# Kernel tuning notes

Hardware: AMD Instinct MI355X
Metric: run time of the kernel (lower is better)

## Reference

```python
import jax, jax.numpy as jnp
import numpy as np

N = 50000
E = 800000
NODE_DIM = 15
HID = 64
HEADS = 4
NEG_SLOPE = 0.2


def _add_self_loops(edge_index, n):
    loops = jnp.arange(n, dtype=edge_index.dtype)
    src = jnp.concatenate([edge_index[0], loops])
    dst = jnp.concatenate([edge_index[1], loops])
    return src, dst


def gat_conv(x, edge_index, W, att_src, att_dst, bias, concat):
    # x: [N, F_in]; W: [F_in, heads*out]; att_*: [heads, out]; bias: [heads*out] or [out]
    n = x.shape[0]
    heads, out_dim = att_src.shape
    src, dst = _add_self_loops(edge_index, n)
    h = (x @ W).reshape(n, heads, out_dim)              # [N, H, D]
    a_src = jnp.sum(h * att_src[None], axis=-1)          # [N, H]
    a_dst = jnp.sum(h * att_dst[None], axis=-1)          # [N, H]
    e = a_src[src] + a_dst[dst]                          # [E', H]
    e = jnp.where(e > 0, e, NEG_SLOPE * e)               # LeakyReLU(0.2)
    # segment softmax over incoming edges of each dst node
    m = jax.ops.segment_max(e, dst, num_segments=n)      # [N, H]
    m = jnp.where(jnp.isfinite(m), m, 0.0)
    w = jnp.exp(e - m[dst])                              # [E', H]
    z = jax.ops.segment_sum(w, dst, num_segments=n)      # [N, H]
    alpha = w / z[dst]                                   # [E', H]
    msg = alpha[:, :, None] * h[src]                     # [E', H, D]
    out = jax.ops.segment_sum(msg, dst, num_segments=n)  # [N, H, D]
    if concat:
        return out.reshape(n, heads * out_dim) + bias
    return out.mean(axis=1) + bias


def setup_inputs() -> dict:
    key = jax.random.key(0)
    ks = jax.random.split(key, 11)
    x = jax.random.normal(ks[0], (N, NODE_DIM), dtype=jnp.float32)
    edge_index = jax.random.randint(ks[1], (2, E), 0, N, dtype=jnp.int64)
    s1 = 1.0 / np.sqrt(NODE_DIM)
    s2 = 1.0 / np.sqrt(HEADS * HID)
    return {
        "x": x,
        "edge_index": edge_index,
        "W1": jax.random.normal(ks[2], (NODE_DIM, HEADS * HID), dtype=jnp.float32) * s1,
        "att_src1": jax.random.normal(ks[3], (HEADS, HID), dtype=jnp.float32) * s2,
        "att_dst1": jax.random.normal(ks[4], (HEADS, HID), dtype=jnp.float32) * s2,
        "b1": jnp.zeros((HEADS * HID,), dtype=jnp.float32),
        "W2": jax.random.normal(ks[5], (HEADS * HID, HID), dtype=jnp.float32) * s2,
        "att_src2": jax.random.normal(ks[6], (1, HID), dtype=jnp.float32) * s2,
        "att_dst2": jax.random.normal(ks[7], (1, HID), dtype=jnp.float32) * s2,
        "b2": jnp.zeros((HID,), dtype=jnp.float32),
    }


def reference(x, edge_index, W1, att_src1, att_dst1, b1, W2, att_src2, att_dst2, b2):
    h = gat_conv(x, edge_index, W1, att_src1, att_dst1, b1, concat=True)   # [N, 256]
    h = jax.nn.elu(h)
    # dropout p=0.2 skipped (eval mode)
    h = gat_conv(h, edge_index, W2, att_src2, att_dst2, b2, concat=True)   # heads=1 -> [N, 64]
    return h.mean(axis=0)                                                   # [64]
```

## Files before the change

### kernel.cpp

```cpp
#include <hip/hip_runtime.h>
#include <hip/hip_fp16.h>

#define NNODES 50000
#define NEDGES 800000
#define NEG_SLOPE 0.2f
#define NTOT (NEDGES + NNODES)
#define NB_NODE ((NNODES + 255) / 256)
#define CHUNK 4096
#define NCHUNK ((NEDGES + CHUNK - 1) / CHUNK)
#define CAPB 4800
#define CNTSTRIDE 16
#define ZPAD (NTOT + 32)

typedef _Float16 half8 __attribute__((ext_vector_type(8)));
typedef _Float16 half4 __attribute__((ext_vector_type(4)));
typedef float f32x4 __attribute__((ext_vector_type(4)));

__global__ void setup_scatter(const float* __restrict__ x, const float* __restrict__ W1,
                              const float* __restrict__ att_src, const float* __restrict__ att_dst,
                              const float* __restrict__ W2,
                              const int* __restrict__ srcs, const int* __restrict__ dsts,
                              int* __restrict__ bucket_cnt, int* __restrict__ bucketbuf,
                              float* __restrict__ x16, float* __restrict__ asrc4,
                              float* __restrict__ adst4, _Float16* __restrict__ W2T) {
    int t = threadIdx.x;
    __shared__ unsigned short meta[CHUNK];
    __shared__ int lcnt[NB_NODE], lbase[NB_NODE];
    __shared__ float swa[16][4], swd[16][4];
    if (blockIdx.x < NCHUNK) {
        int b = blockIdx.x;
        for (int i = t; i < NB_NODE; i += 256) lcnt[i] = 0;
        __syncthreads();
        int e0 = b * CHUNK;
        int e1 = e0 + CHUNK; if (e1 > NEDGES) e1 = NEDGES;
        for (int e = e0 + t; e < e1; e += 256) {
            int d = dsts[e];
            meta[e - e0] = (unsigned short)d;
            atomicAdd(&lcnt[d >> 8], 1);
        }
        __syncthreads();
        for (int i = t; i < NB_NODE; i += 256) {
            int c = lcnt[i];
            lbase[i] = c ? atomicAdd(&bucket_cnt[i * CNTSTRIDE], c) : 0;
        }
        __syncthreads();
        for (int i = t; i < NB_NODE; i += 256) lcnt[i] = 0;
        __syncthreads();
        for (int e = e0 + t; e < e1; e += 256) {
            int dv = meta[e - e0];
            int bk = dv >> 8;
            int pos = lbase[bk] + atomicAdd(&lcnt[bk], 1);
            if (pos < CAPB) bucketbuf[bk * CAPB + pos] = ((dv & 255) << 16) | srcs[e];
        }
    } else {
        int b = blockIdx.x - NCHUNK;
        if (t < 128) {
            int k = (t & 63) >> 2, h = t & 3;
            float s = 0.f;
            if (k < 15) {
                const float* att = (t < 64) ? att_src : att_dst;
#pragma unroll 16
                for (int d = 0; d < 64; ++d)
                    s += W1[k * 256 + h * 64 + d] * att[h * 64 + d];
            }
            if (t < 64) swa[k][h] = s; else swd[k][h] = s;
        }
        int tid = b * 256 + t;
        if (tid < 64 * 256) {
            int n = tid >> 8, k = tid & 255;
            W2T[n * 256 + k] = (_Float16)W2[k * 64 + n];
        }
        __syncthreads();
        int nid = tid;
        if (nid < NNODES) {
            float xv[16];
#pragma unroll
            for (int k = 0; k < 15; ++k) xv[k] = x[nid * 15 + k];
            xv[15] = 0.f;
#pragma unroll
            for (int k = 0; k < 16; k += 4)
                *(float4*)(x16 + (size_t)nid * 16 + k) =
                    make_float4(xv[k], xv[k+1], xv[k+2], xv[k+3]);
            float ps[4] = {0.f, 0.f, 0.f, 0.f}, pd[4] = {0.f, 0.f, 0.f, 0.f};
#pragma unroll
            for (int k = 0; k < 15; ++k)
#pragma unroll
                for (int h = 0; h < 4; ++h) {
                    ps[h] += xv[k] * swa[k][h];
                    pd[h] += xv[k] * swd[k][h];
                }
            *(float4*)(asrc4 + nid * 4) = make_float4(ps[0], ps[1], ps[2], ps[3]);
            *(float4*)(adst4 + nid * 4) = make_float4(pd[0], pd[1], pd[2], pd[3]);
        }
    }
}

__global__ void scanA(const int* __restrict__ bucket_cnt, const int* __restrict__ bucketbuf,
                      int* __restrict__ rowstart, int* __restrict__ partials) {
    int b = blockIdx.x, t = threadIdx.x, lane = t & 63, wid = t >> 6;
    __shared__ int hist[256];
    __shared__ int ws[4];
    int i = b * 256 + t;
    hist[t] = (i < NNODES) ? 1 : 0;
    __syncthreads();
    int n = bucket_cnt[b * CNTSTRIDE]; if (n > CAPB) n = CAPB;
    const int* buf = bucketbuf + (size_t)b * CAPB;
    for (int j = t; j < n; j += 256)
        atomicAdd(&hist[buf[j] >> 16], 1);
    __syncthreads();
    int v = (i < NNODES) ? hist[t] : 0;
    int incl = v;
#pragma unroll
    for (int off = 1; off < 64; off <<= 1) {
        int u = __shfl_up(incl, off, 64);
        if (lane >= off) incl += u;
    }
    if (lane == 63) ws[wid] = incl;
    __syncthreads();
    int w0 = ws[0], w1 = ws[1], w2 = ws[2], w3 = ws[3];
    int woff = (wid > 0 ? w0 : 0) + (wid > 1 ? w1 : 0) + (wid > 2 ? w2 : 0);
    if (i < NNODES) rowstart[i] = woff + (incl - v);
    if (t == 0) partials[b] = w0 + w1 + w2 + w3;
}

__global__ void local_sort(const int* __restrict__ bucket_cnt, const int* __restrict__ bucketbuf,
                           int* __restrict__ rowstart, const int* __restrict__ partials,
                           const float4* __restrict__ asrc4, const float4* __restrict__ adst4,
                           int* __restrict__ srclist, float4* __restrict__ sw4) {
    int b = blockIdx.x, t = threadIdx.x;
    __shared__ int cur[256];
    __shared__ int local[8192];
    __shared__ float4 sadst[256];
    __shared__ int boffs[2];
    if (t < 2) boffs[t] = 0;
    int idx = b * 256 + t;
    int nid = idx;
    int rs0 = rowstart[b * 256];
    int fin0 = (idx < NNODES) ? rowstart[idx] : 0;
    if (nid < NNODES) sadst[t] = adst4[nid];
    __syncthreads();
    if (t < NB_NODE) {
        int v = partials[t];
        if (t < b) atomicAdd(&boffs[0], v);
        atomicAdd(&boffs[1], v);
    }
    if (b == 0 && t == 0) sw4[ZPAD] = make_float4(0.f, 0.f, 0.f, 0.f);
    __syncthreads();
    int boff = boffs[0];
    int base = rs0 + boff;
    int fin = fin0 + boff;
    cur[t] = (idx < NNODES) ? (fin - base) : 0;
    __syncthreads();
    if (nid < NNODES) rowstart[nid] = fin;
    if (b == NB_NODE - 1 && t == 0) rowstart[NNODES] = boffs[1];
    if (nid < NNODES) {
        int pos = atomicAdd(&cur[t], 1);
        local[pos] = (t << 16) | nid;
    }
    int n = bucket_cnt[b * CNTSTRIDE]; if (n > CAPB) n = CAPB;
    const int* buf = bucketbuf + (size_t)b * CAPB;
    for (int i = t; i < n; i += 256) {
        int entry = buf[i];
        int pos = atomicAdd(&cur[entry >> 16], 1);
        local[pos] = entry;
    }
    __syncthreads();
    int total = partials[b];
    for (int i = t; i < total; i += 256) {
        int e = local[i];
        int s = e & 0xFFFF, dl = e >> 16;
        srclist[base + i] = s;
        float4 as = asrc4[s];
        float4 ad = sadst[dl];
        float e0 = as.x + ad.x, e1 = as.y + ad.y, e2 = as.z + ad.z, e3 = as.w + ad.w;
        e0 = fmaxf(e0, NEG_SLOPE * e0); e1 = fmaxf(e1, NEG_SLOPE * e1);
        e2 = fmaxf(e2, NEG_SLOPE * e2); e3 = fmaxf(e3, NEG_SLOPE * e3);
        sw4[base + i] = make_float4(__expf(e0), __expf(e1), __expf(e2), __expf(e3));
    }
}

__global__ __launch_bounds__(256) void layer1_fused(
        const float* __restrict__ x16, const int* __restrict__ rowstart,
        const int* __restrict__ srclist, const float4* __restrict__ sw4,
        const float* __restrict__ W1, const float* __restrict__ b1,
        const _Float16* __restrict__ W2T,
        const float* __restrict__ att_src2, const float* __restrict__ att_dst2,
        __half* __restrict__ h2, float* __restrict__ as2, float* __restrict__ ad2) {
    int wid = threadIdx.x >> 6, lane = threadIdx.x & 63;
    int g = lane >> 4, k = lane & 15;
    int base = blockIdx.x * 16 + wid * 4;
    int nid = base + g;
    int beg = rowstart[nid];
    int cnt = rowstart[nid + 1] - beg;
    int cmax = cnt;
    cmax = max(cmax, __shfl_xor(cmax, 16, 64));
    cmax = max(cmax, __shfl_xor(cmax, 32, 64));
    cmax = __builtin_amdgcn_readfirstlane(cmax);
    int gb = g * 16;
    float4 acc = {0.f, 0.f, 0.f, 0.f};
    float4 zs  = {0.f, 0.f, 0.f, 0.f};
    for (int c0 = 0; c0 < cmax; c0 += 16) {
        int sv = (c0 + k < cnt) ? srclist[beg + c0 + k] : 0;
        int bmax = cmax - c0; if (bmax > 16) bmax = 16;
        for (int j = 0; j < bmax; j += 4) {
            int i0 = c0 + j;
            int s0 = __shfl(sv, gb + j + 0, 64);
            int s1 = __shfl(sv, gb + j + 1, 64);
            int s2 = __shfl(sv, gb + j + 2, 64);
            int s3 = __shfl(sv, gb + j + 3, 64);
            int w0i = (i0 + 0 < cnt) ? beg + i0 + 0 : ZPAD;
            int w1i = (i0 + 1 < cnt) ? beg + i0 + 1 : ZPAD;
            int w2i = (i0 + 2 < cnt) ? beg + i0 + 2 : ZPAD;
            int w3i = (i0 + 3 < cnt) ? beg + i0 + 3 : ZPAD;
            float4 w0 = sw4[w0i];
            float4 w1 = sw4[w1i];
            float4 w2 = sw4[w2i];
            float4 w3 = sw4[w3i];
            float x0 = x16[s0 * 16 + k];
            float x1 = x16[s1 * 16 + k];
            float x2 = x16[s2 * 16 + k];
            float x3 = x16[s3 * 16 + k];
            zs.x += (w0.x + w1.x) + (w2.x + w3.x);
            zs.y += (w0.y + w1.y) + (w2.y + w3.y);
            zs.z += (w0.z + w1.z) + (w2.z + w3.z);
            zs.w += (w0.w + w1.w) + (w2.w + w3.w);
            acc.x = fmaf(w3.x, x3, fmaf(w2.x, x2, fmaf(w1.x, x1, fmaf(w0.x, x0, acc.x))));
            acc.y = fmaf(w3.y, x3, fmaf(w2.y, x2, fmaf(w1.y, x1, fmaf(w0.y, x0, acc.y))));
            acc.z = fmaf(w3.z, x3, fmaf(w2.z, x2, fmaf(w1.z, x1, fmaf(w0.z, x0, acc.z))));
            acc.w = fmaf(w3.w, x3, fmaf(w2.w, x2, fmaf(w1.w, x1, fmaf(w0.w, x0, acc.w))));
        }
    }
    __shared__ float sacc[4][4][64];
    sacc[wid][g][0 * 16 + k] = acc.x / zs.x;
    sacc[wid][g][1 * 16 + k] = acc.y / zs.y;
    sacc[wid][g][2 * 16 + k] = acc.z / zs.z;
    sacc[wid][g][3 * 16 + k] = acc.w / zs.w;
    int c = lane, h2i = c >> 4;
    float4 bo = *(const float4*)(b1 + c * 4);
    float4 o0 = bo, o1 = bo, o2 = bo, o3 = bo;
#pragma unroll
    for (int kk = 0; kk < 15; ++kk) {
        float4 wv = *(const float4*)(W1 + kk * 256 + c * 4);
        float a0 = sacc[wid][0][h2i * 16 + kk];
        float a1 = sacc[wid][1][h2i * 16 + kk];
        float a2 = sacc[wid][2][h2i * 16 + kk];
        float a3 = sacc[wid][3][h2i * 16 + kk];
        o0.x = fmaf(a0, wv.x, o0.x); o0.y = fmaf(a0, wv.y, o0.y);
        o0.z = fmaf(a0, wv.z, o0.z); o0.w = fmaf(a0, wv.w, o0.w);
        o1.x = fmaf(a1, wv.x, o1.x); o1.y = fmaf(a1, wv.y, o1.y);
        o1.z = fmaf(a1, wv.z, o1.z); o1.w = fmaf(a1, wv.w, o1.w);
        o2.x = fmaf(a2, wv.x, o2.x); o2.y = fmaf(a2, wv.y, o2.y);
        o2.z = fmaf(a2, wv.z, o2.z); o2.w = fmaf(a2, wv.w, o2.w);
        o3.x = fmaf(a3, wv.x, o3.x); o3.y = fmaf(a3, wv.y, o3.y);
        o3.z = fmaf(a3, wv.z, o3.z); o3.w = fmaf(a3, wv.w, o3.w);
    }
    __shared__ _Float16 ot[16][264];
    float4 ov[4] = {o0, o1, o2, o3};
#pragma unroll
    for (int gp = 0; gp < 4; ++gp) {
        float p0 = ov[gp].x, p1 = ov[gp].y, p2 = ov[gp].z, p3 = ov[gp].w;
        p0 = p0 > 0.f ? p0 : __expf(p0) - 1.f;
        p1 = p1 > 0.f ? p1 : __expf(p1) - 1.f;
        p2 = p2 > 0.f ? p2 : __expf(p2) - 1.f;
        p3 = p3 > 0.f ? p3 : __expf(p3) - 1.f;
        half4 st;
        st[0] = (_Float16)p0; st[1] = (_Float16)p1;
        st[2] = (_Float16)p2; st[3] = (_Float16)p3;
        *(half4*)&ot[wid * 4 + gp][c * 4] = st;
    }
    __syncthreads();
    int m16 = lane & 15, quad = lane >> 4;
    f32x4 cc = {0.f, 0.f, 0.f, 0.f};
#pragma unroll
    for (int k0 = 0; k0 < 256; k0 += 32) {
        half8 a = *(const half8*)&ot[m16][k0 + quad * 8];
        half8 bf = *(const half8*)(W2T + (size_t)(wid * 16 + m16) * 256 + k0 + quad * 8);
        cc = __builtin_amdgcn_mfma_f32_16x16x32_f16(a, bf, cc, 0, 0, 0);
    }
    __shared__ _Float16 h2t[16][72];
#pragma unroll
    for (int r = 0; r < 4; ++r)
        h2t[quad * 4 + r][wid * 16 + m16] = (_Float16)cc[r];
    __syncthreads();
    int trow = threadIdx.x >> 4, tc = threadIdx.x & 15;
    int rg = blockIdx.x * 16 + trow;
    half4 hval = *(const half4*)&h2t[trow][tc * 4];
    *(half4*)((_Float16*)h2 + (size_t)rg * 64 + tc * 4) = hval;
    float ps = 0.f, pd = 0.f;
#pragma unroll
    for (int j = 0; j < 4; ++j) {
        float v = (float)hval[j];
        ps += v * att_src2[tc * 4 + j];
        pd += v * att_dst2[tc * 4 + j];
    }
    ps += __shfl_xor(ps, 1, 64); ps += __shfl_xor(ps, 2, 64);
    ps += __shfl_xor(ps, 4, 64); ps += __shfl_xor(ps, 8, 64);
    pd += __shfl_xor(pd, 1, 64); pd += __shfl_xor(pd, 2, 64);
    pd += __shfl_xor(pd, 4, 64); pd += __shfl_xor(pd, 8, 64);
    if (tc == 0) { as2[rg] = ps; ad2[rg] = pd; }
}

__global__ void layer2_aggr(const __half* __restrict__ h2, const int* __restrict__ rowstart,
                            const int* __restrict__ srclist,
                            const float* __restrict__ as2, const float* __restrict__ ad2,
                            const float* __restrict__ b2, float* __restrict__ out2) {
    int wid = threadIdx.x >> 6, lane = threadIdx.x & 63;
    int sub = lane >> 5, l2 = lane & 31;
    int nid = blockIdx.x * 8 + wid * 2 + sub;
    int beg = rowstart[nid];
    int cnt = rowstart[nid + 1] - beg;
    int cmax = max(cnt, __shfl_xor(cnt, 32, 64));
    cmax = __builtin_amdgcn_readfirstlane(cmax);
    float ad = ad2[nid];
    const __half2* hp = (const __half2*)h2;
    __half2 acc2 = __float2half2_rn(0.f);
    float zs = 0.f;
    int sb = sub * 32;
    for (int c0 = 0; c0 < cmax; c0 += 32) {
        int sv = (c0 + l2 < cnt) ? srclist[beg + c0 + l2] : 0;
        int bmax = cmax - c0; if (bmax > 32) bmax = 32;
        for (int j = 0; j < bmax; j += 4) {
#pragma unroll
            for (int u = 0; u < 4; ++u) {
                int jj = j + u;
                int s = __shfl(sv, sb + jj, 64);
                bool valid = (c0 + jj) < cnt;
                float e = as2[s] + ad;
                e = fmaxf(e, NEG_SLOPE * e);
                float wv = valid ? __expf(e) : 0.f;
                __half2 gv = hp[s * 32 + l2];
                zs += wv;
                acc2 = __hfma2(__float2half2_rn(wv), gv, acc2);
            }
        }
    }
    float2 f = __half22float2(acc2);
    float rz = 1.f / zs;
    float2 bo = *(const float2*)(b2 + l2 * 2);
    *(float2*)(out2 + (size_t)nid * 64 + l2 * 2) = make_float2(f.x * rz + bo.x,
                                                               f.y * rz + bo.y);
}


__global__ void reduce_kernel(const float* __restrict__ out2, float* __restrict__ dout) {
    int t = threadIdx.x;
    int col = t & 63, sub = t >> 6;
    float acc = 0.f;
    for (int r = blockIdx.x * 4 + sub; r < NNODES; r += 256 * 4)
        acc += out2[r * 64 + col];
    __shared__ float sh[256];
    sh[t] = acc;
    __syncthreads();
    if (t < 64) {
        float v = sh[t] + sh[t + 64] + sh[t + 128] + sh[t + 192];
        atomicAdd(&dout[t], v * (1.0f / NNODES));
    }
}


extern "C" void kernel_launch(void* const* d_in, const int* in_sizes, int n_in,
                              void* d_out, int out_size, void* d_ws, size_t ws_size,
                              hipStream_t stream) {
    const float* x        = (const float*)d_in[0];
    const int*   ei       = (const int*)d_in[1];
    const float* W1       = (const float*)d_in[2];
    const float* att_src1 = (const float*)d_in[3];
    const float* att_dst1 = (const float*)d_in[4];
    const float* b1       = (const float*)d_in[5];
    const float* W2       = (const float*)d_in[6];
    const float* att_src2 = (const float*)d_in[7];
    const float* att_dst2 = (const float*)d_in[8];
    const float* b2       = (const float*)d_in[9];
    float* out = (float*)d_out;

    char* ws = (char*)d_ws;
    size_t off = 0;
    auto take = [&](size_t bytes) -> char* {
        char* p = ws + off;
        off = (off + bytes + 255) & ~(size_t)255;
        return p;
    };
    int*      bucket_cnt = (int*)take((size_t)NB_NODE * CNTSTRIDE * sizeof(int));
    int*      bucketbuf  = (int*)take((size_t)NB_NODE * CAPB * sizeof(int));
    int*      rowstart   = (int*)take((NNODES + 1) * sizeof(int));
    int*      partials   = (int*)take(256 * sizeof(int));
    int*      srclist    = (int*)take(((size_t)NTOT + 64) * sizeof(int));
    float*    sw4        = (float*)take(((size_t)NTOT + 64) * 4 * sizeof(float));
    float*    x16        = (float*)take((size_t)NNODES * 16 * sizeof(float));
    float*    asrc4      = (float*)take((size_t)NNODES * 4 * sizeof(float));
    float*    adst4      = (float*)take((size_t)NNODES * 4 * sizeof(float));
    _Float16* W2T        = (_Float16*)take(64 * 256 * sizeof(_Float16));
    __half*   h2         = (__half*)take((size_t)NNODES * 64 * sizeof(__half));
    float*    as2        = (float*)take((size_t)NNODES * sizeof(float));
    float*    ad2        = (float*)take((size_t)NNODES * sizeof(float));
    float*    out2       = (float*)take((size_t)NNODES * 64 * sizeof(float));

    const int* srcs = ei;
    const int* dsts = ei + NEDGES;

    hipMemsetAsync(d_out, 0, 64 * sizeof(float), stream);
    hipMemsetAsync(bucket_cnt, 0, (size_t)NB_NODE * CNTSTRIDE * sizeof(int), stream);

    setup_scatter<<<NCHUNK + NB_NODE, 256, 0, stream>>>(x, W1, att_src1, att_dst1, W2,
                                                        srcs, dsts, bucket_cnt, bucketbuf,
                                                        x16, asrc4, adst4, W2T);
    scanA<<<NB_NODE, 256, 0, stream>>>(bucket_cnt, bucketbuf, rowstart, partials);
    local_sort<<<NB_NODE, 256, 0, stream>>>(bucket_cnt, bucketbuf, rowstart, partials,
                                            (const float4*)asrc4, (const float4*)adst4,
                                            srclist, (float4*)sw4);

    layer1_fused<<<NNODES / 16, 256, 0, stream>>>(x16, rowstart, srclist, (const float4*)sw4,
                                                  W1, b1, W2T, att_src2, att_dst2,
                                                  h2, as2, ad2);

    layer2_aggr<<<NNODES / 8, 256, 0, stream>>>(h2, rowstart, srclist, as2, ad2, b2, out2);

    reduce_kernel<<<256, 256, 0, stream>>>(out2, out);
}
```

Before: 192.7 us.

## Merge scan and local sort into one kernel and fold output reduction into aggregation

The histogram-scan and local-sort kernels become a single sort kernel. It claims a global output segment with an atomic allocator and stores a per-node (start, count) descriptor instead of a global prefix-sum rowstart, which removes a kernel launch and a round trip through global memory. Layer-2 aggregation now reduces its node outputs into shared memory and atomically adds them into 256 partial rows, so the full N×64 output buffer is never written or re-read. The costs are heavier shared-memory use in the sort kernel and more atomic contention, and bucket segments are no longer in node order.

```diff
diff --git a/kernel.cpp b/kernel.cpp
--- a/kernel.cpp
+++ b/kernel.cpp
@@ -95,20 +95,29 @@
     }
 }
 
-__global__ void scanA(const int* __restrict__ bucket_cnt, const int* __restrict__ bucketbuf,
-                      int* __restrict__ rowstart, int* __restrict__ partials) {
+__global__ void sort_kernel(const int* __restrict__ bucket_cnt, const int* __restrict__ bucketbuf,
+                            const float4* __restrict__ asrc4, const float4* __restrict__ adst4,
+                            int* __restrict__ alloc, int2* __restrict__ row_desc,
+                            int* __restrict__ srclist, float4* __restrict__ sw4) {
     int b = blockIdx.x, t = threadIdx.x, lane = t & 63, wid = t >> 6;
-    __shared__ int hist[256];
-    __shared__ int ws[4];
-    int i = b * 256 + t;
-    hist[t] = (i < NNODES) ? 1 : 0;
+    __shared__ int hist[256], cur[256], ws[4];
+    __shared__ int raw[CAPB];
+    __shared__ int sorted[5120];
+    __shared__ float4 sadst[256];
+    __shared__ int sbase;
+    int nid = b * 256 + t;
+    hist[t] = (nid < NNODES) ? 1 : 0;
+    if (nid < NNODES) sadst[t] = adst4[nid];
+    if (b == 0 && t == 0) sw4[ZPAD] = make_float4(0.f, 0.f, 0.f, 0.f);
     __syncthreads();
     int n = bucket_cnt[b * CNTSTRIDE]; if (n > CAPB) n = CAPB;
-    const int* buf = bucketbuf + (size_t)b * CAPB;
-    for (int j = t; j < n; j += 256)
-        atomicAdd(&hist[buf[j] >> 16], 1);
-    __syncthreads();
-    int v = (i < NNODES) ? hist[t] : 0;
+    for (int i = t; i < n; i += 256) {
+        int e = bucketbuf[(size_t)b * CAPB + i];
+        raw[i] = e;
+        atomicAdd(&hist[e >> 16], 1);
+    }
+    __syncthreads();
+    int v = hist[t];
     int incl = v;
 #pragma unroll
     for (int off = 1; off < 64; off <<= 1) {
@@ -119,55 +128,26 @@
     __syncthreads();
     int w0 = ws[0], w1 = ws[1], w2 = ws[2], w3 = ws[3];
     int woff = (wid > 0 ? w0 : 0) + (wid > 1 ? w1 : 0) + (wid > 2 ? w2 : 0);
-    if (i < NNODES) rowstart[i] = woff + (incl - v);
-    if (t == 0) partials[b] = w0 + w1 + w2 + w3;
-}
-
-__global__ void local_sort(const int* __restrict__ bucket_cnt, const int* __restrict__ bucketbuf,
-                           int* __restrict__ rowstart, const int* __restrict__ partials,
-                           const float4* __restrict__ asrc4, const float4* __restrict__ adst4,
-                           int* __restrict__ srclist, float4* __restrict__ sw4) {
-    int b = blockIdx.x, t = threadIdx.x;
-    __shared__ int cur[256];
-    __shared__ int local[8192];
-    __shared__ float4 sadst[256];
-    __shared__ int boffs[2];
-    if (t < 2) boffs[t] = 0;
-    int idx = b * 256 + t;
-    int nid = idx;
-    int rs0 = rowstart[b * 256];
-    int fin0 = (idx < NNODES) ? rowstart[idx] : 0;
-    if (nid < NNODES) sadst[t] = adst4[nid];
-    __syncthreads();
-    if (t < NB_NODE) {
-        int v = partials[t];
-        if (t < b) atomicAdd(&boffs[0], v);
-        atomicAdd(&boffs[1], v);
-    }
-    if (b == 0 && t == 0) sw4[ZPAD] = make_float4(0.f, 0.f, 0.f, 0.f);
-    __syncthreads();
-    int boff = boffs[0];
-    int base = rs0 + boff;
-    int fin = fin0 + boff;
-    cur[t] = (idx < NNODES) ? (fin - base) : 0;
-    __syncthreads();
-    if (nid < NNODES) rowstart[nid] = fin;
-    if (b == NB_NODE - 1 && t == 0) rowstart[NNODES] = boffs[1];
+    int excl = woff + (incl - v);
+    int totalb = w0 + w1 + w2 + w3;
+    if (t == 0) sbase = atomicAdd(alloc, totalb);
+    __syncthreads();
+    int base = sbase;
+    cur[t] = excl;
+    if (nid < NNODES) row_desc[nid] = make_int2(base + excl, v);
+    __syncthreads();
     if (nid < NNODES) {
         int pos = atomicAdd(&cur[t], 1);
-        local[pos] = (t << 16) | nid;
-    }
-    int n = bucket_cnt[b * CNTSTRIDE]; if (n > CAPB) n = CAPB;
-    const int* buf = bucketbuf + (size_t)b * CAPB;
+        sorted[pos] = (t << 16) | nid;
+    }
     for (int i = t; i < n; i += 256) {
-        int entry = buf[i];
-        int pos = atomicAdd(&cur[entry >> 16], 1);
-        local[pos] = entry;
-    }
-    __syncthreads();
-    int total = partials[b];
-    for (int i = t; i < total; i += 256) {
-        int e = local[i];
+        int e = raw[i];
+        int pos = atomicAdd(&cur[e >> 16], 1);
+        sorted[pos] = e;
+    }
+    __syncthreads();
+    for (int i = t; i < totalb; i += 256) {
+        int e = sorted[i];
         int s = e & 0xFFFF, dl = e >> 16;
         srclist[base + i] = s;
         float4 as = asrc4[s];
@@ -180,7 +160,7 @@
 }
 
 __global__ __launch_bounds__(256) void layer1_fused(
-        const float* __restrict__ x16, const int* __restrict__ rowstart,
+        const float* __restrict__ x16, const int2* __restrict__ row_desc,
         const int* __restrict__ srclist, const float4* __restrict__ sw4,
         const float* __restrict__ W1, const float* __restrict__ b1,
         const _Float16* __restrict__ W2T,
@@ -190,8 +170,8 @@
     int g = lane >> 4, k = lane & 15;
     int base = blockIdx.x * 16 + wid * 4;
     int nid = base + g;
-    int beg = rowstart[nid];
-    int cnt = rowstart[nid + 1] - beg;
+    int2 rd = row_desc[nid];
+    int beg = rd.x, cnt = rd.y;
     int cmax = cnt;
     cmax = max(cmax, __shfl_xor(cmax, 16, 64));
     cmax = max(cmax, __shfl_xor(cmax, 32, 64));
@@ -300,15 +280,17 @@
     if (tc == 0) { as2[rg] = ps; ad2[rg] = pd; }
 }
 
-__global__ void layer2_aggr(const __half* __restrict__ h2, const int* __restrict__ rowstart,
+__global__ void layer2_aggr(const __half* __restrict__ h2, const int2* __restrict__ row_desc,
                             const int* __restrict__ srclist,
                             const float* __restrict__ as2, const float* __restrict__ ad2,
-                            const float* __restrict__ b2, float* __restrict__ out2) {
+                            const float* __restrict__ b2, float* __restrict__ out_partial) {
     int wid = threadIdx.x >> 6, lane = threadIdx.x & 63;
     int sub = lane >> 5, l2 = lane & 31;
     int nid = blockIdx.x * 8 + wid * 2 + sub;
-    int beg = rowstart[nid];
-    int cnt = rowstart[nid + 1] - beg;
+    __shared__ float baccum[64];
+    if (threadIdx.x < 64) baccum[threadIdx.x] = 0.f;
+    int2 rd = row_desc[nid];
+    int beg = rd.x, cnt = rd.y;
     int cmax = max(cnt, __shfl_xor(cnt, 32, 64));
     cmax = __builtin_amdgcn_readfirstlane(cmax);
     float ad = ad2[nid];
@@ -316,6 +298,7 @@
     __half2 acc2 = __float2half2_rn(0.f);
     float zs = 0.f;
     int sb = sub * 32;
+    __syncthreads();
     for (int c0 = 0; c0 < cmax; c0 += 32) {
         int sv = (c0 + l2 < cnt) ? srclist[beg + c0 + l2] : 0;
         int bmax = cmax - c0; if (bmax > 32) bmax = 32;
@@ -337,24 +320,24 @@
     float2 f = __half22float2(acc2);
     float rz = 1.f / zs;
     float2 bo = *(const float2*)(b2 + l2 * 2);
-    *(float2*)(out2 + (size_t)nid * 64 + l2 * 2) = make_float2(f.x * rz + bo.x,
-                                                               f.y * rz + bo.y);
-}
-
-
-__global__ void reduce_kernel(const float* __restrict__ out2, float* __restrict__ dout) {
+    atomicAdd(&baccum[l2 * 2 + 0], f.x * rz + bo.x);
+    atomicAdd(&baccum[l2 * 2 + 1], f.y * rz + bo.y);
+    __syncthreads();
+    if (threadIdx.x < 64)
+        atomicAdd(&out_partial[(blockIdx.x & 255) * 64 + threadIdx.x], baccum[threadIdx.x]);
+}
+
+__global__ void reduce_kernel(const float* __restrict__ out_partial, float* __restrict__ dout) {
     int t = threadIdx.x;
-    int col = t & 63, sub = t >> 6;
+    int col = t & 63, row = t >> 6;
     float acc = 0.f;
-    for (int r = blockIdx.x * 4 + sub; r < NNODES; r += 256 * 4)
-        acc += out2[r * 64 + col];
+    for (int s = row; s < 256; s += 4)
+        acc += out_partial[s * 64 + col];
     __shared__ float sh[256];
     sh[t] = acc;
     __syncthreads();
-    if (t < 64) {
-        float v = sh[t] + sh[t + 64] + sh[t + 128] + sh[t + 192];
-        atomicAdd(&dout[t], v * (1.0f / NNODES));
-    }
+    if (t < 64)
+        dout[t] = (sh[t] + sh[t + 64] + sh[t + 128] + sh[t + 192]) * (1.0f / NNODES);
 }
 
 
@@ -380,10 +363,13 @@
         off = (off + bytes + 255) & ~(size_t)255;
         return p;
     };
-    int*      bucket_cnt = (int*)take((size_t)NB_NODE * CNTSTRIDE * sizeof(int));
+    int*      bucket_cnt  = (int*)take((size_t)NB_NODE * CNTSTRIDE * sizeof(int));
+    int*      alloc       = (int*)take(256);
+    float*    out_partial = (float*)take(256 * 64 * sizeof(float));
+    size_t    zero_bytes  = (size_t)NB_NODE * CNTSTRIDE * sizeof(int) + 256
+                            + 256 * 64 * sizeof(float);
     int*      bucketbuf  = (int*)take((size_t)NB_NODE * CAPB * sizeof(int));
-    int*      rowstart   = (int*)take((NNODES + 1) * sizeof(int));
-    int*      partials   = (int*)take(256 * sizeof(int));
+    int2*     row_desc   = (int2*)take((size_t)NNODES * sizeof(int2));
     int*      srclist    = (int*)take(((size_t)NTOT + 64) * sizeof(int));
     float*    sw4        = (float*)take(((size_t)NTOT + 64) * 4 * sizeof(float));
     float*    x16        = (float*)take((size_t)NNODES * 16 * sizeof(float));
@@ -393,27 +379,25 @@
     __half*   h2         = (__half*)take((size_t)NNODES * 64 * sizeof(__half));
     float*    as2        = (float*)take((size_t)NNODES * sizeof(float));
     float*    ad2        = (float*)take((size_t)NNODES * sizeof(float));
-    float*    out2       = (float*)take((size_t)NNODES * 64 * sizeof(float));
 
     const int* srcs = ei;
     const int* dsts = ei + NEDGES;
 
-    hipMemsetAsync(d_out, 0, 64 * sizeof(float), stream);
-    hipMemsetAsync(bucket_cnt, 0, (size_t)NB_NODE * CNTSTRIDE * sizeof(int), stream);
+    hipMemsetAsync(bucket_cnt, 0, zero_bytes, stream);
 
     setup_scatter<<<NCHUNK + NB_NODE, 256, 0, stream>>>(x, W1, att_src1, att_dst1, W2,
                                                         srcs, dsts, bucket_cnt, bucketbuf,
                                                         x16, asrc4, adst4, W2T);
-    scanA<<<NB_NODE, 256, 0, stream>>>(bucket_cnt, bucketbuf, rowstart, partials);
-    local_sort<<<NB_NODE, 256, 0, stream>>>(bucket_cnt, bucketbuf, rowstart, partials,
-                                            (const float4*)asrc4, (const float4*)adst4,
-                                            srclist, (float4*)sw4);
-
-    layer1_fused<<<NNODES / 16, 256, 0, stream>>>(x16, rowstart, srclist, (const float4*)sw4,
+    sort_kernel<<<NB_NODE, 256, 0, stream>>>(bucket_cnt, bucketbuf,
+                                             (const float4*)asrc4, (const float4*)adst4,
+                                             alloc, row_desc, srclist, (float4*)sw4);
+
+    layer1_fused<<<NNODES / 16, 256, 0, stream>>>(x16, row_desc, srclist, (const float4*)sw4,
                                                   W1, b1, W2T, att_src2, att_dst2,
                                                   h2, as2, ad2);
 
-    layer2_aggr<<<NNODES / 8, 256, 0, stream>>>(h2, rowstart, srclist, as2, ad2, b2, out2);
-
-    reduce_kernel<<<256, 256, 0, stream>>>(out2, out);
-}
+    layer2_aggr<<<NNODES / 8, 256, 0, stream>>>(h2, row_desc, srclist, as2, ad2, b2,
+                                                out_partial);
+
+    reduce_kernel<<<1, 256, 0, stream>>>(out_partial, out);
+}
```

Result: no change. 192.0 us (median of 2 runs) (-0.4%).
